# Performance work log

Hardware: AMD Instinct MI355X
Metric: run time of the kernel (lower is better)

The kernel has to match this reference:

```python
import jax, jax.numpy as jnp
import numpy as np


def _conv(x, w, b, pad):
    # x: (B,C,H,W), w: (O,I,kh,kw), NCHW conv with given padding
    y = jax.lax.conv_general_dilated(x, w, window_strides=(1, 1), padding=pad,
                                     dimension_numbers=('NCHW', 'OIHW', 'NCHW'))
    return y + b[None, :, None, None]


def _frn(x, eps):
    # FilterResponseNorm: normalize by rms over spatial dims (2,3)
    nu2 = jnp.mean(x * x, axis=(2, 3), keepdims=True)
    return x * jax.lax.rsqrt(nu2 + jnp.abs(eps))


def _mish(x):
    return x * jnp.tanh(jax.nn.softplus(x))


def setup_inputs() -> dict:
    key = jax.random.key(0)
    ks = jax.random.split(key, 9)
    B, C, H, W = 4, 256, 64, 64
    C16 = C // 16
    x = jax.random.normal(ks[0], (B, C, H, W), dtype=jnp.float32)
    s = 0.05
    wq = jax.random.normal(ks[1], (C16, C, 1, 3), dtype=jnp.float32) * s
    bq = jax.random.normal(ks[2], (C16,), dtype=jnp.float32) * s
    wk = jax.random.normal(ks[3], (C16, C, 3, 1), dtype=jnp.float32) * s
    bk = jax.random.normal(ks[4], (C16,), dtype=jnp.float32) * s
    wv = jax.random.normal(ks[5], (C, C, 1, 1), dtype=jnp.float32) * s
    bv = jax.random.normal(ks[6], (C,), dtype=jnp.float32) * s
    gamma = jax.random.normal(ks[7], (1,), dtype=jnp.float32) * 0.1
    eps_q = jnp.full((1, C16, 1, 1), 1e-6, dtype=jnp.float32)
    eps_k = jnp.full((1, C16, 1, 1), 1e-6, dtype=jnp.float32)
    return {"x": x, "wq": wq, "bq": bq, "wk": wk, "bk": bk,
            "wv": wv, "bv": bv, "gamma": gamma, "eps_q": eps_q, "eps_k": eps_k}


def reference(x, wq, bq, wk, bk, wv, bv, gamma, eps_q, eps_k):
    B, C, H, W = x.shape
    N = H * W
    # query branch: Conv2d(k=(1,3), pad=(0,1)) -> FRN -> Mish
    q = _mish(_frn(_conv(x, wq, bq, [(0, 0), (1, 1)]), eps_q))  # (B,C16,H,W)
    # key branch: Conv2d(k=(3,1), pad=(1,0)) -> FRN -> Mish
    k = _mish(_frn(_conv(x, wk, bk, [(1, 1), (0, 0)]), eps_k))  # (B,C16,H,W)
    q = q.reshape(B, -1, N)  # (B,C16,N)
    k = k.reshape(B, -1, N)  # (B,C16,N)
    # affinity[b,n,m] = sum_c q[b,c,n] * k[b,c,m]; softmax over m
    affinity = jnp.einsum('bcn,bcm->bnm', q, k)
    affinity = jax.nn.softmax(affinity, axis=-1)  # (B,N,N)
    v = _conv(x, wv, bv, [(0, 0), (0, 0)]).reshape(B, C, N)  # (B,C,N)
    # weights = v @ affinity^T : weights[b,c,j] = sum_n v[b,c,n] * affinity[b,j,n]
    weights = jnp.einsum('bcn,bjn->bcj', v, affinity).reshape(B, C, H, W)
    return gamma * weights + x
```

## Files before the change

kernel.cpp:

```cpp
#include <hip/hip_runtime.h>
#include <stdint.h>

#define NB 4
#define CC 256
#define C16 16
#define HH 64
#define WW 64
#define NN 4096

typedef __attribute__((ext_vector_type(8))) short short8;
typedef __attribute__((ext_vector_type(4))) float floatx4;
typedef __attribute__((ext_vector_type(16))) float floatx16;

#if __has_builtin(__builtin_amdgcn_exp2f)
#define EXP2(x) __builtin_amdgcn_exp2f(x)
#else
#define EXP2(x) exp2f(x)
#endif

__device__ __forceinline__ unsigned short f2bf(float f) {
    union { float f; unsigned u; } v; v.f = f;
    unsigned r = v.u + 0x7fffu + ((v.u >> 16) & 1u);
    return (unsigned short)(r >> 16);
}
__device__ __forceinline__ float bf2f(unsigned short h) {
    union { unsigned u; float f; } v; v.u = (unsigned)h << 16;
    return v.f;
}


__global__ __launch_bounds__(256) void prep_kernel(
        const float* __restrict__ x, const float* __restrict__ wv,
        const float* __restrict__ wq, const float* __restrict__ wk,
        unsigned short* __restrict__ xT, unsigned short* __restrict__ wvb,
        unsigned short* __restrict__ wqkb, float* __restrict__ nu2) {
    int bid = blockIdx.x;
    if (bid < 1024) {
        __shared__ float tile_t[64][65];
        int nt = bid & 63, ct = (bid >> 6) & 3, b = bid >> 8;
        int n0 = nt * 64, c0 = ct * 64;
        int tid = threadIdx.x;
        int rg = tid >> 4, f = tid & 15;
        const float* xb = x + ((size_t)b * CC + c0) * NN + n0;
#pragma unroll
        for (int p = 0; p < 4; ++p) {
            int c = p * 16 + rg;
            float4 v = *(const float4*)(xb + (size_t)c * NN + f * 4);
            tile_t[f * 4 + 0][c] = v.x;
            tile_t[f * 4 + 1][c] = v.y;
            tile_t[f * 4 + 2][c] = v.z;
            tile_t[f * 4 + 3][c] = v.w;
        }
        __syncthreads();
        unsigned short* xtb = xT + ((size_t)b * NN + n0) * CC + c0;
#pragma unroll
        for (int p = 0; p < 4; ++p) {
            int n = p * 16 + rg;
            ushort4 st;
            st.x = f2bf(tile_t[n][f * 4 + 0]);
            st.y = f2bf(tile_t[n][f * 4 + 1]);
            st.z = f2bf(tile_t[n][f * 4 + 2]);
            st.w = f2bf(tile_t[n][f * 4 + 3]);
            *(ushort4*)(xtb + (size_t)n * CC + f * 4) = st;
        }
    } else {
        int idx = (bid - 1024) * 256 + threadIdx.x;
        if (bid == 1024 && threadIdx.x < 128) nu2[threadIdx.x] = 0.f;
        if (idx < 16384) {
            float4 v = *(const float4*)(wv + idx * 4);
            ushort4 o;
            o.x = f2bf(v.x); o.y = f2bf(v.y); o.z = f2bf(v.z); o.w = f2bf(v.w);
            *(ushort4*)(wvb + idx * 4) = o;
        } else if (idx < 16384 + 6144) {
            int base = (idx - 16384) * 4;
#pragma unroll
            for (int u = 0; u < 4; ++u) {
                int e = base + u;
                int t = e / 12288;
                int i = e - t * 12288;
                int tap = i >> 12, o = (i >> 8) & 15, c = i & 255;
                const float* src = t ? wk : wq;
                wqkb[e] = f2bf(src[o * 768 + c * 3 + tap]);
            }
        }
    }
}

__global__ __launch_bounds__(256) void conv_kernel(
        const unsigned short* __restrict__ xT, const unsigned short* __restrict__ wvb,
        const unsigned short* __restrict__ wqkb, const float* __restrict__ bv,
        const float* __restrict__ bq, const float* __restrict__ bk,
        unsigned short* __restrict__ vb, unsigned short* __restrict__ qrawh,
        unsigned short* __restrict__ krawh, float* __restrict__ nu2) {
    int bid = blockIdx.x;
    int tid = threadIdx.x;
    int wv_ = tid >> 6, lane = tid & 63;
    int q16 = lane >> 4, c16 = lane & 15;
    if (bid < 512) {
        int ntile = bid & 63, b = (bid >> 6) & 3, ch = bid >> 8;
        int n0 = ntile * 64;
        int cb = ch * 128 + wv_ * 32;
        floatx4 fzero = {0.f, 0.f, 0.f, 0.f};
        floatx4 acc[2][4];
        for (int ct = 0; ct < 2; ++ct)
            for (int nt = 0; nt < 4; ++nt) acc[ct][nt] = fzero;
        const unsigned short* xb = xT + ((size_t)b * NN + n0) * CC;
        for (int kc = 0; kc < 8; ++kc) {
            int ko = kc * 32 + q16 * 8;
            short8 a0 = *(const short8*)(wvb + (size_t)(cb + c16) * CC + ko);
            short8 a1 = *(const short8*)(wvb + (size_t)(cb + 16 + c16) * CC + ko);
            short8 bf[4];
#pragma unroll
            for (int nt = 0; nt < 4; ++nt)
                bf[nt] = *(const short8*)(xb + (size_t)(nt * 16 + c16) * CC + ko);
#pragma unroll
            for (int nt = 0; nt < 4; ++nt) {
                acc[0][nt] = __builtin_amdgcn_mfma_f32_16x16x32_bf16(bf[nt], a0, acc[0][nt], 0, 0, 0);
                acc[1][nt] = __builtin_amdgcn_mfma_f32_16x16x32_bf16(bf[nt], a1, acc[1][nt], 0, 0, 0);
            }
        }
        float bv0 = bv[cb + c16], bv1 = bv[cb + 16 + c16];
        int off = 32 * 8 * (q16 >> 1) + (q16 & 1) * 4 + c16 * 8;
#pragma unroll
        for (int ct = 0; ct < 2; ++ct) {
            float bvv = ct ? bv1 : bv0;
#pragma unroll
            for (int nt = 0; nt < 4; ++nt) {
                size_t fb = (((size_t)b * 8 + ch * 4 + wv_) * 256 + (n0 >> 4) + nt) * 512;
                ushort4 st;
                st.x = f2bf(acc[ct][nt][0] + bvv);
                st.y = f2bf(acc[ct][nt][1] + bvv);
                st.z = f2bf(acc[ct][nt][2] + bvv);
                st.w = f2bf(acc[ct][nt][3] + bvv);
                *(ushort4*)(vb + fb + off + ct * 16 * 8) = st;
            }
        }
    } else {
        int cv = bid - 512;
        int nb2 = cv & 63, b = cv >> 6;
        int nl = nb2 * 64 + wv_ * 16 + c16;
        int h = nl >> 6, w = nl & 63;
        bool vm1 = (w != 0), vp1 = (w != 63);
        bool vm64 = (h != 0), vp64 = (h != 63);
        short8 zero8 = {0, 0, 0, 0, 0, 0, 0, 0};
        floatx4 accq = {0.f, 0.f, 0.f, 0.f}, acck = {0.f, 0.f, 0.f, 0.f};
        const unsigned short* xb = xT + (size_t)b * NN * CC;
        const unsigned short* wrow = wqkb + c16 * 256;
        for (int kc = 0; kc < 8; ++kc) {
            int ko = kc * 32 + q16 * 8;
            short8 b0 = *(const short8*)(xb + (size_t)nl * CC + ko);
            short8 bm1 = vm1 ? *(const short8*)(xb + (size_t)(nl - 1) * CC + ko) : zero8;
            short8 bp1 = vp1 ? *(const short8*)(xb + (size_t)(nl + 1) * CC + ko) : zero8;
            short8 bm64 = vm64 ? *(const short8*)(xb + (size_t)(nl - 64) * CC + ko) : zero8;
            short8 bp64 = vp64 ? *(const short8*)(xb + (size_t)(nl + 64) * CC + ko) : zero8;
            short8 aq0 = *(const short8*)(wrow + 0 * 4096 + ko);
            short8 aq1 = *(const short8*)(wrow + 1 * 4096 + ko);
            short8 aq2 = *(const short8*)(wrow + 2 * 4096 + ko);
            short8 ak0 = *(const short8*)(wrow + 12288 + 0 * 4096 + ko);
            short8 ak1 = *(const short8*)(wrow + 12288 + 1 * 4096 + ko);
            short8 ak2 = *(const short8*)(wrow + 12288 + 2 * 4096 + ko);
            accq = __builtin_amdgcn_mfma_f32_16x16x32_bf16(bm1, aq0, accq, 0, 0, 0);
            accq = __builtin_amdgcn_mfma_f32_16x16x32_bf16(b0, aq1, accq, 0, 0, 0);
            accq = __builtin_amdgcn_mfma_f32_16x16x32_bf16(bp1, aq2, accq, 0, 0, 0);
            acck = __builtin_amdgcn_mfma_f32_16x16x32_bf16(bm64, ak0, acck, 0, 0, 0);
            acck = __builtin_amdgcn_mfma_f32_16x16x32_bf16(b0, ak1, acck, 0, 0, 0);
            acck = __builtin_amdgcn_mfma_f32_16x16x32_bf16(bp64, ak2, acck, 0, 0, 0);
        }
        int nst = nb2 * 64 + wv_ * 16 + q16 * 4;
        float bqv = bq[c16], bkv = bk[c16];
        ushort4 sq4, sk4;
        float ssq = 0.f, ssk = 0.f;
        {
            float vq0 = accq[0] + bqv, vq1 = accq[1] + bqv, vq2 = accq[2] + bqv, vq3 = accq[3] + bqv;
            float vk0 = acck[0] + bkv, vk1 = acck[1] + bkv, vk2 = acck[2] + bkv, vk3 = acck[3] + bkv;
            sq4.x = f2bf(vq0); sq4.y = f2bf(vq1); sq4.z = f2bf(vq2); sq4.w = f2bf(vq3);
            sk4.x = f2bf(vk0); sk4.y = f2bf(vk1); sk4.z = f2bf(vk2); sk4.w = f2bf(vk3);
            ssq = vq0 * vq0 + vq1 * vq1 + vq2 * vq2 + vq3 * vq3;
            ssk = vk0 * vk0 + vk1 * vk1 + vk2 * vk2 + vk3 * vk3;
        }
        *(ushort4*)(qrawh + (size_t)(b * C16 + c16) * NN + nst) = sq4;
        *(ushort4*)(krawh + (size_t)(b * C16 + c16) * NN + nst) = sk4;
        ssq += __shfl_xor(ssq, 16, 64);
        ssq += __shfl_xor(ssq, 32, 64);
        ssk += __shfl_xor(ssk, 16, 64);
        ssk += __shfl_xor(ssk, 32, 64);
        if (lane < 16) {
            atomicAdd(nu2 + b * C16 + lane, ssq);
            atomicAdd(nu2 + 64 + b * C16 + lane, ssk);
        }
    }
}

__global__ __launch_bounds__(256) void frn_mish_kernel(
        const unsigned short* __restrict__ qrawh, const unsigned short* __restrict__ krawh,
        const float* __restrict__ nu2, const float* __restrict__ eps_q,
        const float* __restrict__ eps_k, unsigned short* __restrict__ qb,
        unsigned short* __restrict__ kb) {
    int blk = blockIdx.x;
    int tensor = blk >> 8;
    int b = (blk >> 6) & 3;
    int nch = blk & 63;
    const unsigned short* raw = tensor ? krawh : qrawh;
    const float* eps = tensor ? eps_k : eps_q;
    unsigned short* outp = tensor ? kb : qb;
    const float* nu = nu2 + tensor * 64 + b * C16;
    float scale = tensor ? 1.0f : 1.44269504f;
    int n = nch * 64 + (threadIdx.x & 63);
    int oq = threadIdx.x >> 6;
    ushort4 pk4;
#pragma unroll
    for (int i = 0; i < 4; ++i) {
        int o = oq * 4 + i;
        float r = bf2f(raw[(size_t)(b * C16 + o) * NN + n]);
        float v = r * rsqrtf(nu[o] * (1.f / (float)NN) + fabsf(eps[o]));
        float sp = fmaxf(v, 0.f) + log1pf(expf(-fabsf(v)));
        float m = v * tanhf(sp) * scale;
        ((unsigned short*)&pk4)[i] = f2bf(m);
    }
    size_t base = ((size_t)b * 128 + (n >> 5)) * 512 + (size_t)(n & 31) * 8
                + (size_t)(oq >> 1) * 256 + (oq & 1) * 4;
    *(ushort4*)(outp + base) = pk4;
}

__device__ __forceinline__ void pack_p0(
        floatx16 sc, short8* A0, short8* A1, float* lsum) {
    unsigned pk[8];
    float ls = 0.f;
#pragma unroll
    for (int p = 0; p < 8; ++p) {
        float e0 = EXP2(sc[2 * p]);
        float e1 = EXP2(sc[2 * p + 1]);
        ls += e0 + e1;
        pk[p] = __builtin_amdgcn_perm(__float_as_uint(e1), __float_as_uint(e0), 0x07060302u);
    }
    *lsum += ls;
    asm("v_permlane32_swap_b32 %0, %1" : "+v"(pk[0]), "+v"(pk[2]));
    asm("v_permlane32_swap_b32 %0, %1" : "+v"(pk[1]), "+v"(pk[3]));
    asm("v_permlane32_swap_b32 %0, %1" : "+v"(pk[4]), "+v"(pk[6]));
    asm("v_permlane32_swap_b32 %0, %1" : "+v"(pk[5]), "+v"(pk[7]));
    union { unsigned u[4]; short8 s; } a0, a1;
    a0.u[0] = pk[0]; a0.u[1] = pk[1]; a0.u[2] = pk[2]; a0.u[3] = pk[3];
    a1.u[0] = pk[4]; a1.u[1] = pk[5]; a1.u[2] = pk[6]; a1.u[3] = pk[7];
    *A0 = a0.s; *A1 = a1.s;
}

__global__ __launch_bounds__(256, 2) void attn_kernel(
        const unsigned short* __restrict__ qb, const unsigned short* __restrict__ kb,
        const unsigned short* __restrict__ vb, const float* __restrict__ x,
        const float* __restrict__ gamma_p, float* __restrict__ out) {
    __shared__ float lpart[4][2][32];
    __shared__ float obuf[4][32][33];

    int tid = threadIdx.x;
    int wv_ = __builtin_amdgcn_readfirstlane(tid >> 6);
    int lane = tid & 63;
    int l31 = lane & 31, lh = lane >> 5;
    int id = blockIdx.x;
    int cs = id & 1, b = (id >> 1) & 3, jt = id >> 3;
    int jbase = jt * 64, cb = cs * 128;
    int lane8 = lane * 8;

    const unsigned short* qfb = qb + ((size_t)b * 128 + (jbase >> 5)) * 512 + lane8;
    const unsigned short* kfb = kb + ((size_t)b * 128 + (wv_ * 32)) * 512 + lane8;

    short8 qf0 = *(const short8*)qfb;
    short8 qf1 = *(const short8*)(qfb + 512);

    floatx16 z16 = {0,0,0,0,0,0,0,0,0,0,0,0,0,0,0,0};
    floatx16 acc0[4], acc1[4];
#pragma unroll
    for (int cg = 0; cg < 4; ++cg) { acc0[cg] = z16; acc1[cg] = z16; }
    float lsum0 = 0.f, lsum1 = 0.f;

    const unsigned short* vp0 = vb + (((size_t)b * 8 + cs * 4 + 0) * 256 + wv_ * 64) * 512 + lane8;
    const unsigned short* vp1 = vb + (((size_t)b * 8 + cs * 4 + 1) * 256 + wv_ * 64) * 512 + lane8;
    const unsigned short* vp2 = vb + (((size_t)b * 8 + cs * 4 + 2) * 256 + wv_ * 64) * 512 + lane8;
    const unsigned short* vp3 = vb + (((size_t)b * 8 + cs * 4 + 3) * 256 + wv_ * 64) * 512 + lane8;

    short8 ak = *(const short8*)kfb;
#pragma unroll 1
    for (int step = 0; step < 32; ++step) {
        short8 vf0a = *(const short8*)vp0, vf0b = *(const short8*)(vp0 + 512);
        short8 vf1a = *(const short8*)vp1, vf1b = *(const short8*)(vp1 + 512);
        short8 vf2a = *(const short8*)vp2, vf2b = *(const short8*)(vp2 + 512);
        short8 vf3a = *(const short8*)vp3, vf3b = *(const short8*)(vp3 + 512);
        floatx16 sc0 = __builtin_amdgcn_mfma_f32_32x32x16_bf16(ak, qf0, z16, 0, 0, 0);
        floatx16 sc1 = __builtin_amdgcn_mfma_f32_32x32x16_bf16(ak, qf1, z16, 0, 0, 0);
        ak = *(const short8*)(kfb + (size_t)((step + 1) & 31) * 512);
        short8 A00, A01, A10, A11;
        pack_p0(sc0, &A00, &A01, &lsum0);
        pack_p0(sc1, &A10, &A11, &lsum1);
        __builtin_amdgcn_s_setprio(1);
        acc0[0] = __builtin_amdgcn_mfma_f32_32x32x16_bf16(A00, vf0a, acc0[0], 0, 0, 0);
        acc0[0] = __builtin_amdgcn_mfma_f32_32x32x16_bf16(A01, vf0b, acc0[0], 0, 0, 0);
        acc1[0] = __builtin_amdgcn_mfma_f32_32x32x16_bf16(A10, vf0a, acc1[0], 0, 0, 0);
        acc1[0] = __builtin_amdgcn_mfma_f32_32x32x16_bf16(A11, vf0b, acc1[0], 0, 0, 0);
        acc0[1] = __builtin_amdgcn_mfma_f32_32x32x16_bf16(A00, vf1a, acc0[1], 0, 0, 0);
        acc0[1] = __builtin_amdgcn_mfma_f32_32x32x16_bf16(A01, vf1b, acc0[1], 0, 0, 0);
        acc1[1] = __builtin_amdgcn_mfma_f32_32x32x16_bf16(A10, vf1a, acc1[1], 0, 0, 0);
        acc1[1] = __builtin_amdgcn_mfma_f32_32x32x16_bf16(A11, vf1b, acc1[1], 0, 0, 0);
        acc0[2] = __builtin_amdgcn_mfma_f32_32x32x16_bf16(A00, vf2a, acc0[2], 0, 0, 0);
        acc0[2] = __builtin_amdgcn_mfma_f32_32x32x16_bf16(A01, vf2b, acc0[2], 0, 0, 0);
        acc1[2] = __builtin_amdgcn_mfma_f32_32x32x16_bf16(A10, vf2a, acc1[2], 0, 0, 0);
        acc1[2] = __builtin_amdgcn_mfma_f32_32x32x16_bf16(A11, vf2b, acc1[2], 0, 0, 0);
        acc0[3] = __builtin_amdgcn_mfma_f32_32x32x16_bf16(A00, vf3a, acc0[3], 0, 0, 0);
        acc0[3] = __builtin_amdgcn_mfma_f32_32x32x16_bf16(A01, vf3b, acc0[3], 0, 0, 0);
        acc1[3] = __builtin_amdgcn_mfma_f32_32x32x16_bf16(A10, vf3a, acc1[3], 0, 0, 0);
        acc1[3] = __builtin_amdgcn_mfma_f32_32x32x16_bf16(A11, vf3b, acc1[3], 0, 0, 0);
        __builtin_amdgcn_s_setprio(0);
        vp0 += 1024; vp1 += 1024; vp2 += 1024; vp3 += 1024;
    }

    lsum0 += __shfl_xor(lsum0, 32, 64);
    lsum1 += __shfl_xor(lsum1, 32, 64);
    if (lh == 0) { lpart[wv_][0][l31] = lsum0; lpart[wv_][1][l31] = lsum1; }
    __syncthreads();

    int j31 = tid & 31;
    float gamma = gamma_p[0];
    float gl0 = gamma / (lpart[0][0][j31] + lpart[1][0][j31] + lpart[2][0][j31] + lpart[3][0][j31]);
    float gl1 = gamma / (lpart[0][1][j31] + lpart[1][1][j31] + lpart[2][1][j31] + lpart[3][1][j31]);
    const float* xbb = x + (size_t)b * CC * NN;
    float* obb = out + (size_t)b * CC * NN;
    int hofs = lh * 4;
    int cgrp = tid >> 5;
#pragma unroll
    for (int jg = 0; jg < 2; ++jg) {
        float gl = jg ? gl1 : gl0;
#pragma unroll
        for (int cg = 0; cg < 4; ++cg) {
            __syncthreads();
            const floatx16& a = jg ? acc1[cg] : acc0[cg];
#pragma unroll
            for (int r = 0; r < 16; ++r) {
                int row = (r & 3) + 8 * (r >> 2) + hofs;
                obuf[wv_][row][l31] = a[r];
            }
            __syncthreads();
#pragma unroll
            for (int i = 0; i < 4; ++i) {
                int c = cgrp * 4 + i;
                float val = obuf[0][j31][c] + obuf[1][j31][c] + obuf[2][j31][c] + obuf[3][j31][c];
                size_t oidx = (size_t)(cb + cg * 32 + c) * NN + jbase + jg * 32 + j31;
                obb[oidx] = fmaf(gl, val, xbb[oidx]);
            }
        }
    }
}

extern "C" void kernel_launch(void* const* d_in, const int* in_sizes, int n_in,
                              void* d_out, int out_size, void* d_ws, size_t ws_size,
                              hipStream_t stream) {
    const float* x     = (const float*)d_in[0];
    const float* wq    = (const float*)d_in[1];
    const float* bq    = (const float*)d_in[2];
    const float* wk    = (const float*)d_in[3];
    const float* bk    = (const float*)d_in[4];
    const float* wv    = (const float*)d_in[5];
    const float* bv    = (const float*)d_in[6];
    const float* gamma = (const float*)d_in[7];
    const float* eps_q = (const float*)d_in[8];
    const float* eps_k = (const float*)d_in[9];
    float* out = (float*)d_out;

    char* ws = (char*)d_ws;
    unsigned short* qrawh = (unsigned short*)ws;
    unsigned short* krawh = (unsigned short*)(ws + (1u << 20));
    float* nu2  = (float*)(ws + (2u << 20));
    unsigned short* qb = (unsigned short*)(ws + (2u << 20) + 4096);
    unsigned short* kb = qb + (size_t)NB * NN * C16;
    unsigned short* vb = kb + (size_t)NB * NN * C16;
    unsigned short* xT = vb + (size_t)NB * CC * NN;
    unsigned short* wvb = xT + (size_t)NB * NN * CC;
    unsigned short* wqkb = wvb + (size_t)CC * CC;

    prep_kernel<<<dim3(1112), dim3(256), 0, stream>>>(x, wv, wq, wk, xT, wvb, wqkb, nu2);
    conv_kernel<<<dim3(768), dim3(256), 0, stream>>>(xT, wvb, wqkb, bv, bq, bk, vb, qrawh, krawh, nu2);
    frn_mish_kernel<<<dim3(512), dim3(256), 0, stream>>>(qrawh, krawh, nu2, eps_q, eps_k, qb, kb);
    attn_kernel<<<dim3(512), dim3(256), 0, stream>>>(qb, kb, vb, x, gamma, out);
}
```

Baseline: 164.5 us.

## Halve attention query tile, double grid, and pipeline score MFMA ahead

Each attention block now handles 32 query columns instead of 64, so the grid doubles to 1024 blocks and the launch bound asks for 3 blocks per CU. This cuts per-thread accumulator registers. The score MFMA for the next key tile is now issued before the current tile's PV MFMAs, overlapping softmax packing with the matrix work. The cost is that each V tile is reused by half as many queries, which doubles total V loads from cache and memory. The larger grid may also leave a partial last wave.

Measured after the change: 175.7 us. 6.8% more time.

```diff
diff --git a/kernel.cpp b/kernel.cpp
--- a/kernel.cpp
+++ b/kernel.cpp
@@ -244,11 +244,11 @@
     *A0 = a0.s; *A1 = a1.s;
 }
 
-__global__ __launch_bounds__(256, 2) void attn_kernel(
+__global__ __launch_bounds__(256, 3) void attn_kernel(
         const unsigned short* __restrict__ qb, const unsigned short* __restrict__ kb,
         const unsigned short* __restrict__ vb, const float* __restrict__ x,
         const float* __restrict__ gamma_p, float* __restrict__ out) {
-    __shared__ float lpart[4][2][32];
+    __shared__ float lpart[4][32];
     __shared__ float obuf[4][32][33];
 
     int tid = threadIdx.x;
@@ -257,20 +257,19 @@
     int l31 = lane & 31, lh = lane >> 5;
     int id = blockIdx.x;
     int cs = id & 1, b = (id >> 1) & 3, jt = id >> 3;
-    int jbase = jt * 64, cb = cs * 128;
+    int jbase = jt * 32, cb = cs * 128;
     int lane8 = lane * 8;
 
-    const unsigned short* qfb = qb + ((size_t)b * 128 + (jbase >> 5)) * 512 + lane8;
+    const unsigned short* qfb = qb + ((size_t)b * 128 + jt) * 512 + lane8;
     const unsigned short* kfb = kb + ((size_t)b * 128 + (wv_ * 32)) * 512 + lane8;
 
-    short8 qf0 = *(const short8*)qfb;
-    short8 qf1 = *(const short8*)(qfb + 512);
+    short8 qf = *(const short8*)qfb;
 
     floatx16 z16 = {0,0,0,0,0,0,0,0,0,0,0,0,0,0,0,0};
-    floatx16 acc0[4], acc1[4];
-#pragma unroll
-    for (int cg = 0; cg < 4; ++cg) { acc0[cg] = z16; acc1[cg] = z16; }
-    float lsum0 = 0.f, lsum1 = 0.f;
+    floatx16 acc[4];
+#pragma unroll
+    for (int cg = 0; cg < 4; ++cg) acc[cg] = z16;
+    float lsum = 0.f;
 
     const unsigned short* vp0 = vb + (((size_t)b * 8 + cs * 4 + 0) * 256 + wv_ * 64) * 512 + lane8;
     const unsigned short* vp1 = vb + (((size_t)b * 8 + cs * 4 + 1) * 256 + wv_ * 64) * 512 + lane8;
@@ -278,72 +277,59 @@
     const unsigned short* vp3 = vb + (((size_t)b * 8 + cs * 4 + 3) * 256 + wv_ * 64) * 512 + lane8;
 
     short8 ak = *(const short8*)kfb;
+    floatx16 sc = __builtin_amdgcn_mfma_f32_32x32x16_bf16(ak, qf, z16, 0, 0, 0);
+    short8 ak2 = *(const short8*)(kfb + 512);
+
 #pragma unroll 1
     for (int step = 0; step < 32; ++step) {
         short8 vf0a = *(const short8*)vp0, vf0b = *(const short8*)(vp0 + 512);
         short8 vf1a = *(const short8*)vp1, vf1b = *(const short8*)(vp1 + 512);
         short8 vf2a = *(const short8*)vp2, vf2b = *(const short8*)(vp2 + 512);
         short8 vf3a = *(const short8*)vp3, vf3b = *(const short8*)(vp3 + 512);
-        floatx16 sc0 = __builtin_amdgcn_mfma_f32_32x32x16_bf16(ak, qf0, z16, 0, 0, 0);
-        floatx16 sc1 = __builtin_amdgcn_mfma_f32_32x32x16_bf16(ak, qf1, z16, 0, 0, 0);
-        ak = *(const short8*)(kfb + (size_t)((step + 1) & 31) * 512);
-        short8 A00, A01, A10, A11;
-        pack_p0(sc0, &A00, &A01, &lsum0);
-        pack_p0(sc1, &A10, &A11, &lsum1);
+        short8 A0, A1;
+        pack_p0(sc, &A0, &A1, &lsum);
+        sc = __builtin_amdgcn_mfma_f32_32x32x16_bf16(ak2, qf, z16, 0, 0, 0);
+        ak2 = *(const short8*)(kfb + (size_t)((step + 2) & 31) * 512);
         __builtin_amdgcn_s_setprio(1);
-        acc0[0] = __builtin_amdgcn_mfma_f32_32x32x16_bf16(A00, vf0a, acc0[0], 0, 0, 0);
-        acc0[0] = __builtin_amdgcn_mfma_f32_32x32x16_bf16(A01, vf0b, acc0[0], 0, 0, 0);
-        acc1[0] = __builtin_amdgcn_mfma_f32_32x32x16_bf16(A10, vf0a, acc1[0], 0, 0, 0);
-        acc1[0] = __builtin_amdgcn_mfma_f32_32x32x16_bf16(A11, vf0b, acc1[0], 0, 0, 0);
-        acc0[1] = __builtin_amdgcn_mfma_f32_32x32x16_bf16(A00, vf1a, acc0[1], 0, 0, 0);
-        acc0[1] = __builtin_amdgcn_mfma_f32_32x32x16_bf16(A01, vf1b, acc0[1], 0, 0, 0);
-        acc1[1] = __builtin_amdgcn_mfma_f32_32x32x16_bf16(A10, vf1a, acc1[1], 0, 0, 0);
-        acc1[1] = __builtin_amdgcn_mfma_f32_32x32x16_bf16(A11, vf1b, acc1[1], 0, 0, 0);
-        acc0[2] = __builtin_amdgcn_mfma_f32_32x32x16_bf16(A00, vf2a, acc0[2], 0, 0, 0);
-        acc0[2] = __builtin_amdgcn_mfma_f32_32x32x16_bf16(A01, vf2b, acc0[2], 0, 0, 0);
-        acc1[2] = __builtin_amdgcn_mfma_f32_32x32x16_bf16(A10, vf2a, acc1[2], 0, 0, 0);
-        acc1[2] = __builtin_amdgcn_mfma_f32_32x32x16_bf16(A11, vf2b, acc1[2], 0, 0, 0);
-        acc0[3] = __builtin_amdgcn_mfma_f32_32x32x16_bf16(A00, vf3a, acc0[3], 0, 0, 0);
-        acc0[3] = __builtin_amdgcn_mfma_f32_32x32x16_bf16(A01, vf3b, acc0[3], 0, 0, 0);
-        acc1[3] = __builtin_amdgcn_mfma_f32_32x32x16_bf16(A10, vf3a, acc1[3], 0, 0, 0);
-        acc1[3] = __builtin_amdgcn_mfma_f32_32x32x16_bf16(A11, vf3b, acc1[3], 0, 0, 0);
+        acc[0] = __builtin_amdgcn_mfma_f32_32x32x16_bf16(A0, vf0a, acc[0], 0, 0, 0);
+        acc[0] = __builtin_amdgcn_mfma_f32_32x32x16_bf16(A1, vf0b, acc[0], 0, 0, 0);
+        acc[1] = __builtin_amdgcn_mfma_f32_32x32x16_bf16(A0, vf1a, acc[1], 0, 0, 0);
+        acc[1] = __builtin_amdgcn_mfma_f32_32x32x16_bf16(A1, vf1b, acc[1], 0, 0, 0);
+        acc[2] = __builtin_amdgcn_mfma_f32_32x32x16_bf16(A0, vf2a, acc[2], 0, 0, 0);
+        acc[2] = __builtin_amdgcn_mfma_f32_32x32x16_bf16(A1, vf2b, acc[2], 0, 0, 0);
+        acc[3] = __builtin_amdgcn_mfma_f32_32x32x16_bf16(A0, vf3a, acc[3], 0, 0, 0);
+        acc[3] = __builtin_amdgcn_mfma_f32_32x32x16_bf16(A1, vf3b, acc[3], 0, 0, 0);
         __builtin_amdgcn_s_setprio(0);
         vp0 += 1024; vp1 += 1024; vp2 += 1024; vp3 += 1024;
     }
 
-    lsum0 += __shfl_xor(lsum0, 32, 64);
-    lsum1 += __shfl_xor(lsum1, 32, 64);
-    if (lh == 0) { lpart[wv_][0][l31] = lsum0; lpart[wv_][1][l31] = lsum1; }
+    lsum += __shfl_xor(lsum, 32, 64);
+    if (lh == 0) lpart[wv_][l31] = lsum;
     __syncthreads();
 
     int j31 = tid & 31;
     float gamma = gamma_p[0];
-    float gl0 = gamma / (lpart[0][0][j31] + lpart[1][0][j31] + lpart[2][0][j31] + lpart[3][0][j31]);
-    float gl1 = gamma / (lpart[0][1][j31] + lpart[1][1][j31] + lpart[2][1][j31] + lpart[3][1][j31]);
+    float gl = gamma / (lpart[0][j31] + lpart[1][j31] + lpart[2][j31] + lpart[3][j31]);
     const float* xbb = x + (size_t)b * CC * NN;
     float* obb = out + (size_t)b * CC * NN;
     int hofs = lh * 4;
     int cgrp = tid >> 5;
 #pragma unroll
-    for (int jg = 0; jg < 2; ++jg) {
-        float gl = jg ? gl1 : gl0;
-#pragma unroll
-        for (int cg = 0; cg < 4; ++cg) {
-            __syncthreads();
-            const floatx16& a = jg ? acc1[cg] : acc0[cg];
-#pragma unroll
-            for (int r = 0; r < 16; ++r) {
-                int row = (r & 3) + 8 * (r >> 2) + hofs;
-                obuf[wv_][row][l31] = a[r];
-            }
-            __syncthreads();
-#pragma unroll
-            for (int i = 0; i < 4; ++i) {
-                int c = cgrp * 4 + i;
-                float val = obuf[0][j31][c] + obuf[1][j31][c] + obuf[2][j31][c] + obuf[3][j31][c];
-                size_t oidx = (size_t)(cb + cg * 32 + c) * NN + jbase + jg * 32 + j31;
-                obb[oidx] = fmaf(gl, val, xbb[oidx]);
-            }
+    for (int cg = 0; cg < 4; ++cg) {
+        __syncthreads();
+        const floatx16& a = acc[cg];
+#pragma unroll
+        for (int r = 0; r < 16; ++r) {
+            int row = (r & 3) + 8 * (r >> 2) + hofs;
+            obuf[wv_][row][l31] = a[r];
+        }
+        __syncthreads();
+#pragma unroll
+        for (int i = 0; i < 4; ++i) {
+            int c = cgrp * 4 + i;
+            float val = obuf[0][j31][c] + obuf[1][j31][c] + obuf[2][j31][c] + obuf[3][j31][c];
+            size_t oidx = (size_t)(cb + cg * 32 + c) * NN + jbase + j31;
+            obb[oidx] = fmaf(gl, val, xbb[oidx]);
         }
     }
 }
@@ -377,5 +363,5 @@
     prep_kernel<<<dim3(1112), dim3(256), 0, stream>>>(x, wv, wq, wk, xT, wvb, wqkb, nu2);
     conv_kernel<<<dim3(768), dim3(256), 0, stream>>>(xT, wvb, wqkb, bv, bq, bk, vb, qrawh, krawh, nu2);
     frn_mish_kernel<<<dim3(512), dim3(256), 0, stream>>>(qrawh, krawh, nu2, eps_q, eps_k, qb, kb);
-    attn_kernel<<<dim3(512), dim3(256), 0, stream>>>(qb, kb, vb, x, gamma, out);
-}
+    attn_kernel<<<dim3(1024), dim3(256), 0, stream>>>(qb, kb, vb, x, gamma, out);
+}
```
